# Kernel optimization log

Measured on AMD Instinct MI355X. Metric: run time of the kernel, lower is better.

The kernel has to match this reference:

```python
import jax, jax.numpy as jnp
import numpy as np

B, S, K, H = 512, 128, 4, 128  # batch, seq_len, interest_num, hidden_size
ROUTING_TIMES = 3
EPS = 1e-9


def setup_inputs() -> dict:
    key = jax.random.key(0)
    k1, k2 = jax.random.split(key)
    item_eb = jax.random.normal(k1, (B, S, H), dtype=jnp.float32)
    mask = jnp.ones((B, S), dtype=jnp.float32)
    # learned bilinear map parameter (bilinear_type == 2)
    w = jax.random.normal(k2, (1, S, K * H, H), dtype=jnp.float32) * 0.02
    return {"item_eb": item_eb, "mask": mask, "w": w}


def _squash(cap):
    # cap: [B, K, 1, H]
    n = jnp.sum(cap * cap, axis=-1, keepdims=True)
    return (n / (1.0 + n) / jnp.sqrt(n + EPS)) * cap


def reference(item_eb, mask, w):
    # bilinear_type==2: sum(w[:, :S] * item_eb[:, :, None, :], axis=3)
    # expressed as an einsum to avoid the [B,S,K*H,H] intermediate
    item_eb_hat = jnp.einsum('bsh,sdh->bsd', item_eb, w[0])          # [B, S, K*H]
    item_eb_hat = item_eb_hat.reshape(B, S, K, H).transpose(0, 2, 1, 3)  # [B, K, S, H]
    hat_iter = jax.lax.stop_gradient(item_eb_hat)  # stop_grad=True

    atten_mask = jnp.broadcast_to(mask[:, None, :], (B, K, S))
    capsule_weight = jnp.zeros((B, K, S), dtype=item_eb.dtype)  # bilinear_type > 0

    interest_capsule = None
    for i in range(ROUTING_TIMES):
        # torch F.softmax with implicit dim on a 3D tensor -> dim=0 (legacy)
        sw = jax.nn.softmax(capsule_weight, axis=0)
        sw = jnp.where(atten_mask == 0, 0.0, sw)[:, :, None, :]  # [B, K, 1, S]
        src = hat_iter if i < 2 else item_eb_hat
        interest_capsule = _squash(jnp.matmul(sw, src))  # [B, K, 1, H]
        if i < 2:
            delta = jnp.matmul(hat_iter, interest_capsule.transpose(0, 1, 3, 2))  # [B,K,S,1]
            capsule_weight = capsule_weight + delta.reshape(B, K, S)

    return interest_capsule.reshape(B, K, H)
```

## Files before the change

### kernel.cpp

```cpp
#include <hip/hip_runtime.h>
#include <math.h>

#define BB 512
#define SS 128
#define KK 4
#define HH 128
#define DD 512

typedef __attribute__((ext_vector_type(8))) short bf16x8;
typedef __attribute__((ext_vector_type(4))) float f32x4;

__device__ __forceinline__ unsigned short f2bf(float f) {
  unsigned u = __float_as_uint(f);
  unsigned r = u + 0x7fffu + ((u >> 16) & 1u);
  return (unsigned short)(r >> 16);
}
__device__ __forceinline__ ushort4 f2bf4(float4 v) {
  ushort4 o; o.x = f2bf(v.x); o.y = f2bf(v.y); o.z = f2bf(v.z); o.w = f2bf(v.w);
  return o;
}
__device__ __forceinline__ float bfhi(unsigned u) { return __uint_as_float(u & 0xffff0000u); }
__device__ __forceinline__ float bflo(unsigned u) { return __uint_as_float(u << 16); }

__global__ __launch_bounds__(256) void einsum_mfma(
    const float* __restrict__ item,
    const float* __restrict__ w,
    unsigned short* __restrict__ hat)
{
  __shared__ unsigned short Al[128 * 128];
  __shared__ unsigned short Wl[2][128 * 64];
  const int s  = blockIdx.x;
  const int b0 = blockIdx.y * 128;
  const int t  = threadIdx.x;
  const int lane = t & 63, wvq = t >> 6;
  const int qm = wvq & 1, qn = wvq >> 1;
  const int n16 = lane & 15, kq = lane >> 4;

  const float* Abase = item + ((size_t)b0 * SS + s) * HH;
  const float* Wbase = w + (size_t)s * DD * HH;

  const int ac = t & 31, ar0 = t >> 5;
  const int wc = t & 15, wr0 = t >> 4;
  float4 apre[16];
  #pragma unroll
  for (int j = 0; j < 16; ++j)
    apre[j] = *(const float4*)(Abase + (size_t)(ar0 + 8 * j) * (SS * HH) + ac * 4);
  float4 wpre[8];
  #pragma unroll
  for (int j = 0; j < 8; ++j)
    wpre[j] = *(const float4*)(Wbase + (size_t)(wr0 + 16 * j) * HH + wc * 4);

  #pragma unroll
  for (int j = 0; j < 16; ++j) {
    const int r = ar0 + 8 * j;
    const int lg = ac >> 1;
    *(ushort4*)&Al[r * 128 + ((lg ^ (r & 15)) * 8) + (ac & 1) * 4] = f2bf4(apre[j]);
  }
  #pragma unroll
  for (int j = 0; j < 8; ++j) {
    const int r = wr0 + 16 * j;
    *(ushort4*)&Wl[0][r * 64 + ((((wc >> 1) + r) & 7) * 8) + (wc & 1) * 4] = f2bf4(wpre[j]);
  }
  __syncthreads();

  int buf = 0;
  for (int dt = 0; dt < 4; ++dt) {
    f32x4 acc[4][4] = {};
    #pragma unroll
    for (int hs = 0; hs < 2; ++hs) {
      const int step = dt * 2 + hs;
      if (step < 7) {
        const int d0n = ((step + 1) >> 1) * 128;
        const int ksn = ((step + 1) & 1) * 64;
        #pragma unroll
        for (int j = 0; j < 8; ++j)
          wpre[j] = *(const float4*)(Wbase + (size_t)(d0n + wr0 + 16 * j) * HH + ksn + wc * 4);
      }
      #pragma unroll
      for (int kk = 0; kk < 2; ++kk) {
        bf16x8 af[4], bfr[4];
        #pragma unroll
        for (int i = 0; i < 4; ++i) {
          const int ra = qm * 64 + i * 16 + n16;
          const int rb = qn * 64 + i * 16 + n16;
          af[i]  = *(const bf16x8*)&Wl[buf][ra * 64 + ((kk * 4 + kq + ra) & 7) * 8];
          bfr[i] = *(const bf16x8*)&Al[rb * 128 + (((hs * 8 + kk * 4 + kq) ^ (rb & 15)) * 8)];
        }
        #pragma unroll
        for (int i = 0; i < 4; ++i)
          #pragma unroll
          for (int j = 0; j < 4; ++j)
            acc[i][j] = __builtin_amdgcn_mfma_f32_16x16x32_bf16(af[i], bfr[j], acc[i][j], 0, 0, 0);
      }
      if (step < 7) {
        #pragma unroll
        for (int j = 0; j < 8; ++j) {
          const int r = wr0 + 16 * j;
          *(ushort4*)&Wl[buf ^ 1][r * 64 + ((((wc >> 1) + r) & 7) * 8) + (wc & 1) * 4] = f2bf4(wpre[j]);
        }
        __syncthreads();
        buf ^= 1;
      }
    }
    #pragma unroll
    for (int j = 0; j < 4; ++j) {
      const int b = b0 + qn * 64 + j * 16 + n16;
      unsigned short* orow = hat + (((size_t)b * KK + dt) * SS + s) * HH;
      #pragma unroll
      for (int i = 0; i < 4; ++i) {
        const int h = qm * 64 + i * 16 + kq * 4;
        ushort4 o;
        o.x = f2bf(acc[i][j][0]); o.y = f2bf(acc[i][j][1]);
        o.z = f2bf(acc[i][j][2]); o.w = f2bf(acc[i][j][3]);
        *(ushort4*)(orow + h) = o;
      }
    }
  }
}

__global__ __launch_bounds__(256) void softmax_k(
    const float* __restrict__ cw,
    const float* __restrict__ mask,
    float* __restrict__ sw)
{
  __shared__ float rbuf[4];
  const int s = blockIdx.x, k = blockIdx.y, t = threadIdx.x;
  const size_t base = ((size_t)k * SS + s) * BB;
  float v0 = cw[base + t], v1 = cw[base + 256 + t];
  float m = fmaxf(v0, v1);
  #pragma unroll
  for (int o = 32; o; o >>= 1) m = fmaxf(m, __shfl_xor(m, o));
  if ((t & 63) == 0) rbuf[t >> 6] = m;
  __syncthreads();
  m = fmaxf(fmaxf(rbuf[0], rbuf[1]), fmaxf(rbuf[2], rbuf[3]));
  float e0 = expf(v0 - m), e1 = expf(v1 - m);
  float ssum = e0 + e1;
  #pragma unroll
  for (int o = 32; o; o >>= 1) ssum += __shfl_xor(ssum, o);
  __syncthreads();
  if ((t & 63) == 0) rbuf[t >> 6] = ssum;
  __syncthreads();
  float inv = 1.f / (rbuf[0] + rbuf[1] + rbuf[2] + rbuf[3]);
  float m0 = mask[(size_t)t * SS + s];
  float m1 = mask[(size_t)(t + 256) * SS + s];
  sw[(size_t)t * (KK * SS) + k * SS + s]         = (m0 == 0.f) ? 0.f : e0 * inv;
  sw[(size_t)(t + 256) * (KK * SS) + k * SS + s] = (m1 == 0.f) ? 0.f : e1 * inv;
}

__global__ __launch_bounds__(64, 2) void routing_k(
    const unsigned short* __restrict__ hat,
    const float* __restrict__ mask,
    const float* __restrict__ sw_in,
    float* __restrict__ cw,
    float* __restrict__ out, int mode)
{
  __shared__ float sw_l[128];
  __shared__ float red[32][65];
  const int b = blockIdx.x, k = blockIdx.y;
  const int l = threadIdx.x;

  const unsigned* slab = (const unsigned*)(hat + ((size_t)(b * KK + k) * SS) * HH);
  unsigned hp[128];
  #pragma unroll
  for (int s = 0; s < 128; ++s) hp[s] = slab[s * 64 + l];

  if (mode == 0) {
    float2 mv = ((const float2*)(mask + (size_t)b * SS))[l];
    sw_l[2 * l]     = (mv.x == 0.f) ? 0.f : (1.f / 512.f);
    sw_l[2 * l + 1] = (mv.y == 0.f) ? 0.f : (1.f / 512.f);
  } else {
    float2 sv = ((const float2*)(sw_in + ((size_t)b * KK + k) * SS))[l];
    sw_l[2 * l] = sv.x; sw_l[2 * l + 1] = sv.y;
  }
  __syncthreads();

  float c0 = 0.f, c1 = 0.f;
  #pragma unroll
  for (int s = 0; s < 128; ++s) {
    float wv = sw_l[s];
    c0 = fmaf(wv, bflo(hp[s]), c0);
    c1 = fmaf(wv, bfhi(hp[s]), c1);
  }
  float sq = c0 * c0 + c1 * c1;
  #pragma unroll
  for (int o = 32; o; o >>= 1) sq += __shfl_xor(sq, o);
  const float fac = sq / (1.f + sq) / sqrtf(sq + 1e-9f);
  c0 *= fac; c1 *= fac;

  if (mode == 2) {
    ((float2*)(out + ((size_t)b * KK + k) * HH))[l] = make_float2(c0, c1);
    return;
  }

  #pragma unroll
  for (int c = 0; c < 4; ++c) {
    #pragma unroll
    for (int j = 0; j < 32; ++j) {
      const int s = c * 32 + j;
      red[j][l] = fmaf(bflo(hp[s]), c0, bfhi(hp[s]) * c1);
    }
    __syncthreads();
    const int sp = l >> 1, half = l & 1;
    float dsum = 0.f;
    #pragma unroll
    for (int q = 0; q < 32; ++q) dsum += red[sp][half * 32 + q];
    dsum += __shfl_xor(dsum, 1);
    if (half == 0) {
      float* p = cw + ((size_t)k * SS + c * 32 + sp) * BB + b;
      if (mode == 0) *p = dsum; else *p += dsum;
    }
    __syncthreads();
  }
}

extern "C" void kernel_launch(void* const* d_in, const int* in_sizes, int n_in,
                              void* d_out, int out_size, void* d_ws, size_t ws_size,
                              hipStream_t stream) {
  const float* item_eb = (const float*)d_in[0];
  const float* mask    = (const float*)d_in[1];
  const float* w       = (const float*)d_in[2];
  float* out = (float*)d_out;

  char* ws = (char*)d_ws;
  unsigned short* hat_bf = (unsigned short*)ws;
  float* cw  = (float*)(ws + 67108864);
  float* swb = (float*)(ws + 68157440);

  einsum_mfma<<<dim3(128, 4), 256, 0, stream>>>(item_eb, w, hat_bf);

  routing_k<<<dim3(BB, KK), 64, 0, stream>>>(hat_bf, mask, nullptr, cw, out, 0);
  softmax_k<<<dim3(SS, KK), 256, 0, stream>>>(cw, mask, swb);
  routing_k<<<dim3(BB, KK), 64, 0, stream>>>(hat_bf, mask, swb, cw, out, 1);
  softmax_k<<<dim3(SS, KK), 256, 0, stream>>>(cw, mask, swb);
  routing_k<<<dim3(BB, KK), 64, 0, stream>>>(hat_bf, mask, swb, cw, out, 2);
}
```

Baseline: 194.5 us.

## Split routing kernel across two waves to halve per-thread register slab

The routing kernel now runs 128 threads per (batch, interest) block. Each of the two waves holds half of the 128 sequence rows in registers, so the per-thread slab drops from 128 to 64 registers. Partial capsule sums are combined through shared memory with one barrier. The delta reduction is done per wave on its own rows, which removes the per-chunk block barriers. This is meant to raise occupancy and latency hiding on the memory-bound passes over the bf16 hat tensor. In exchange it relies on wave-local LDS ordering without explicit barriers and uses a larger shared reduction buffer.

Result: no change. 197.1 us (+1.3%).

```diff
diff --git a/kernel.cpp b/kernel.cpp
--- a/kernel.cpp
+++ b/kernel.cpp
@@ -147,7 +147,7 @@
   sw[(size_t)(t + 256) * (KK * SS) + k * SS + s] = (m1 == 0.f) ? 0.f : e1 * inv;
 }
 
-__global__ __launch_bounds__(64, 2) void routing_k(
+__global__ __launch_bounds__(128, 4) void routing_k(
     const unsigned short* __restrict__ hat,
     const float* __restrict__ mask,
     const float* __restrict__ sw_in,
@@ -155,32 +155,46 @@
     float* __restrict__ out, int mode)
 {
   __shared__ float sw_l[128];
-  __shared__ float red[32][65];
+  __shared__ float2 part[2][64];
+  __shared__ float red[64][65];
   const int b = blockIdx.x, k = blockIdx.y;
-  const int l = threadIdx.x;
+  const int t = threadIdx.x;
+  const int wv = t >> 6, l = t & 63;
+
+  float2 swv = make_float2(0.f, 0.f);
+  if (l < 32) {
+    const int idx = 32 * wv + l;
+    swv = (mode == 0) ? ((const float2*)(mask + (size_t)b * SS))[idx]
+                      : ((const float2*)(sw_in + ((size_t)b * KK + k) * SS))[idx];
+  }
 
   const unsigned* slab = (const unsigned*)(hat + ((size_t)(b * KK + k) * SS) * HH);
-  unsigned hp[128];
-  #pragma unroll
-  for (int s = 0; s < 128; ++s) hp[s] = slab[s * 64 + l];
-
-  if (mode == 0) {
-    float2 mv = ((const float2*)(mask + (size_t)b * SS))[l];
-    sw_l[2 * l]     = (mv.x == 0.f) ? 0.f : (1.f / 512.f);
-    sw_l[2 * l + 1] = (mv.y == 0.f) ? 0.f : (1.f / 512.f);
-  } else {
-    float2 sv = ((const float2*)(sw_in + ((size_t)b * KK + k) * SS))[l];
-    sw_l[2 * l] = sv.x; sw_l[2 * l + 1] = sv.y;
-  }
-  __syncthreads();
+  unsigned hp[64];
+  #pragma unroll
+  for (int j = 0; j < 64; ++j) hp[j] = slab[(64 * wv + j) * 64 + l];
+
+  if (l < 32) {
+    const int s0 = 64 * wv + 2 * l;
+    if (mode == 0) {
+      sw_l[s0]     = (swv.x == 0.f) ? 0.f : (1.f / 512.f);
+      sw_l[s0 + 1] = (swv.y == 0.f) ? 0.f : (1.f / 512.f);
+    } else {
+      sw_l[s0] = swv.x; sw_l[s0 + 1] = swv.y;
+    }
+  }
 
   float c0 = 0.f, c1 = 0.f;
   #pragma unroll
-  for (int s = 0; s < 128; ++s) {
-    float wv = sw_l[s];
-    c0 = fmaf(wv, bflo(hp[s]), c0);
-    c1 = fmaf(wv, bfhi(hp[s]), c1);
-  }
+  for (int j = 0; j < 64; ++j) {
+    float ww = sw_l[64 * wv + j];
+    c0 = fmaf(ww, bflo(hp[j]), c0);
+    c1 = fmaf(ww, bfhi(hp[j]), c1);
+  }
+  part[wv][l] = make_float2(c0, c1);
+  __syncthreads();
+  float2 o2 = part[wv ^ 1][l];
+  c0 += o2.x; c1 += o2.y;
+
   float sq = c0 * c0 + c1 * c1;
   #pragma unroll
   for (int o = 32; o; o >>= 1) sq += __shfl_xor(sq, o);
@@ -188,28 +202,25 @@
   c0 *= fac; c1 *= fac;
 
   if (mode == 2) {
-    ((float2*)(out + ((size_t)b * KK + k) * HH))[l] = make_float2(c0, c1);
+    if (wv == 0)
+      ((float2*)(out + ((size_t)b * KK + k) * HH))[l] = make_float2(c0, c1);
     return;
   }
 
   #pragma unroll
-  for (int c = 0; c < 4; ++c) {
-    #pragma unroll
-    for (int j = 0; j < 32; ++j) {
-      const int s = c * 32 + j;
-      red[j][l] = fmaf(bflo(hp[s]), c0, bfhi(hp[s]) * c1);
-    }
-    __syncthreads();
+  for (int c = 0; c < 2; ++c) {
+    #pragma unroll
+    for (int j = 0; j < 32; ++j)
+      red[32 * wv + j][l] = fmaf(bflo(hp[c * 32 + j]), c0, bfhi(hp[c * 32 + j]) * c1);
     const int sp = l >> 1, half = l & 1;
     float dsum = 0.f;
     #pragma unroll
-    for (int q = 0; q < 32; ++q) dsum += red[sp][half * 32 + q];
+    for (int q = 0; q < 32; ++q) dsum += red[32 * wv + sp][half * 32 + q];
     dsum += __shfl_xor(dsum, 1);
     if (half == 0) {
-      float* p = cw + ((size_t)k * SS + c * 32 + sp) * BB + b;
+      float* p = cw + ((size_t)k * SS + 64 * wv + c * 32 + sp) * BB + b;
       if (mode == 0) *p = dsum; else *p += dsum;
     }
-    __syncthreads();
   }
 }
 
@@ -228,9 +239,9 @@
 
   einsum_mfma<<<dim3(128, 4), 256, 0, stream>>>(item_eb, w, hat_bf);
 
-  routing_k<<<dim3(BB, KK), 64, 0, stream>>>(hat_bf, mask, nullptr, cw, out, 0);
+  routing_k<<<dim3(BB, KK), 128, 0, stream>>>(hat_bf, mask, nullptr, cw, out, 0);
   softmax_k<<<dim3(SS, KK), 256, 0, stream>>>(cw, mask, swb);
-  routing_k<<<dim3(BB, KK), 64, 0, stream>>>(hat_bf, mask, swb, cw, out, 1);
+  routing_k<<<dim3(BB, KK), 128, 0, stream>>>(hat_bf, mask, swb, cw, out, 1);
   softmax_k<<<dim3(SS, KK), 256, 0, stream>>>(cw, mask, swb);
-  routing_k<<<dim3(BB, KK), 64, 0, stream>>>(hat_bf, mask, swb, cw, out, 2);
-}
+  routing_k<<<dim3(BB, KK), 128, 0, stream>>>(hat_bf, mask, swb, cw, out, 2);
+}
```
